# Kernel optimization log

Measured on AMD Instinct MI355X. Metric: run time of the kernel, lower is better.

Reference implementation:

```python
import jax, jax.numpy as jnp
import numpy as np

N = 8192          # mesh vertices
E = 49152         # directed edges (avg degree 6)
M = 25            # kernel_size per pseudo-dim
DIM = 3           # pseudo-coordinate dim
K = M ** DIM      # 15625 weight matrices per layer
S = 2 ** DIM      # 8 nonzero degree-1 B-spline products per edge
LC, UC = -0.22703196, 0.36853024   # curvature range
LM, UM = 1.2585511, 1.648841       # myelin range
R = 10.0
LAYER_DIMS = [(2, 32), (32, 64), (64, 64), (64, 32), (32, 1)]


def transform(x):
    # rescale curv/myelin channels into [-R, R] with clamping (matches torch masking)
    t0 = (x[:, 0] - LC) / (UC - LC) * (2.0 * R) - R
    t1 = (x[:, 1] - LM) / (UM - LM) * (2.0 * R) - R
    return jnp.stack([jnp.clip(t0, -R, R), jnp.clip(t1, -R, R)], axis=1)


def spline_basis(pseudo):
    # open B-spline, degree 1: v in [0, M-1); 8 corner products per edge
    v = pseudo * (M - 1)
    lo = jnp.floor(v)
    f = v - lo                                                    # [E, DIM]
    lo = lo.astype(jnp.int32)
    bits = (jnp.arange(S)[:, None] >> jnp.arange(DIM)[None, :]) & 1   # [S, DIM]
    oh = bits.astype(pseudo.dtype)
    basis = jnp.prod(oh[None] * f[:, None, :] + (1.0 - oh[None]) * (1.0 - f[:, None, :]), axis=-1)  # [E, S]
    strides = (M ** jnp.arange(DIM)).astype(jnp.int32)
    wi = jnp.sum((lo[:, None, :] + bits[None]) * strides[None, None, :], axis=-1)  # [E, S] kernel indices
    return basis, wi


def spline_conv(h, src, dst, basis, wi, W, root, bias):
    xj = h[src]                                             # [E, Fin] gather
    msg = jnp.zeros((xj.shape[0], W.shape[2]), h.dtype)
    for s in range(S):                                      # fixed 8-way basis loop
        msg = msg + basis[:, s, None] * jnp.einsum('ei,eio->eo', xj, W[wi[:, s]])
    agg = jax.ops.segment_sum(msg, dst, num_segments=N)     # scatter-sum (norm=False)
    return agg + h @ root + bias


def setup_inputs() -> dict:
    key = jax.random.key(0)
    ks = jax.random.split(key, 3 + 2 * len(LAYER_DIMS))
    inp = {
        "x": jax.random.normal(ks[0], (N, 2), dtype=jnp.float32),
        "edge_index": jax.random.randint(ks[1], (2, E), 0, N),
        "pseudo": jax.random.uniform(ks[2], (E, DIM), dtype=jnp.float32),
    }
    for i, (fi, fo) in enumerate(LAYER_DIMS):
        kw, kr = ks[3 + 2 * i], ks[4 + 2 * i]
        inp[f"W{i+1}"] = jax.random.normal(kw, (K, fi, fo), dtype=jnp.float32) / np.float32(np.sqrt(fi * S))
        inp[f"root{i+1}"] = jax.random.normal(kr, (fi, fo), dtype=jnp.float32) / np.float32(np.sqrt(fi))
        inp[f"b{i+1}"] = jnp.zeros((fo,), dtype=jnp.float32)
    return inp


def reference(x, edge_index, pseudo, W1, root1, b1, W2, root2, b2, W3, root3, b3,
              W4, root4, b4, W5, root5, b5):
    src, dst = edge_index[0], edge_index[1]
    basis, wi = spline_basis(pseudo)   # shared across all 5 layers, as in the torch model
    h = transform(x)
    for W, r, b in ((W1, root1, b1), (W2, root2, b2), (W3, root3, b3),
                    (W4, root4, b4), (W5, root5, b5)):
        h = jax.nn.elu(spline_conv(h, src, dst, basis, wi, W, r, b))
    return h.reshape(-1)
```

## Files before the change

### kernel.cpp

```cpp
#include <hip/hip_runtime.h>
#include <math.h>

#define NV 8192
#define EV 49152
#define KK 15625

typedef __attribute__((ext_vector_type(8))) short bf16x8;
typedef __attribute__((ext_vector_type(4))) float f32x4;

__device__ __forceinline__ unsigned short bf16rne(float x) {
    unsigned u = __float_as_uint(x);
    unsigned r = u + 0x7FFFu + ((u >> 16) & 1u);
    return (unsigned short)(r >> 16);
}
__device__ __forceinline__ float bf16tof(unsigned short h) {
    return __uint_as_float(((unsigned)h) << 16);
}

__device__ __forceinline__ void edge_frac(const float* __restrict__ pseudo, int e,
                                          float f[3], int lo[3]) {
#pragma unroll
    for (int j = 0; j < 3; ++j) {
        float v = pseudo[e * 3 + j] * 24.0f;
        float fl = floorf(v);
        int l = (int)fl;
        l = l < 0 ? 0 : (l > 23 ? 23 : l);
        lo[j] = l;
        f[j] = v - (float)l;
    }
}

__global__ void prep_kernel(const float* __restrict__ x, float* __restrict__ h0,
                            int* __restrict__ counts, float* __restrict__ agg) {
    int gt = blockIdx.x * blockDim.x + threadIdx.x;
    if (gt < NV) {
        const float LC = -0.22703196f, UC = 0.36853024f;
        const float LM = 1.2585511f, UM = 1.648841f;
        const float R = 10.0f;
        float t0 = (x[gt * 2 + 0] - LC) / (UC - LC) * (2.0f * R) - R;
        float t1 = (x[gt * 2 + 1] - LM) / (UM - LM) * (2.0f * R) - R;
        h0[gt * 2 + 0] = fminf(fmaxf(t0, -R), R);
        h0[gt * 2 + 1] = fminf(fmaxf(t1, -R), R);
    }
    if (gt < KK) counts[gt] = 0;
    if (gt < NV * 64) agg[gt] = 0.0f;
}

__global__ void hist_kernel(const float* __restrict__ pseudo, int* __restrict__ counts) {
    int e = blockIdx.x * blockDim.x + threadIdx.x;
    if (e >= EV) return;
    float f[3]; int lo[3];
    edge_frac(pseudo, e, f, lo);
#pragma unroll
    for (int s = 0; s < 8; ++s) {
        int wi = (lo[0] + (s & 1)) + 25 * (lo[1] + ((s >> 1) & 1)) + 625 * (lo[2] + ((s >> 2) & 1));
        atomicAdd(&counts[wi], 1);
    }
}

__global__ void scan_kernel(const int* __restrict__ counts, int* __restrict__ offsets,
                            int* __restrict__ cursor) {
    __shared__ int sums[256];
    const int CH = 62;
    int t = threadIdx.x;
    int base = t * CH;
    int s = 0;
    for (int i = 0; i < CH; ++i) {
        int idx = base + i;
        if (idx < KK) s += counts[idx];
    }
    sums[t] = s;
    __syncthreads();
    for (int d = 1; d < 256; d <<= 1) {
        int v = (t >= d) ? sums[t - d] : 0;
        __syncthreads();
        sums[t] += v;
        __syncthreads();
    }
    int run = (t > 0) ? sums[t - 1] : 0;
    for (int i = 0; i < CH; ++i) {
        int idx = base + i;
        if (idx < KK) {
            offsets[idx] = run;
            cursor[idx] = run;
            run += counts[idx];
        }
    }
    if (t == 255) offsets[KK] = run;
}

__global__ void scatter_kernel(const float* __restrict__ pseudo, const int* __restrict__ ei,
                               int* __restrict__ cursor,
                               int2* __restrict__ pair_sb, int* __restrict__ pair_dst) {
    int e = blockIdx.x * blockDim.x + threadIdx.x;
    if (e >= EV) return;
    float f[3]; int lo[3];
    edge_frac(pseudo, e, f, lo);
    int src = ei[e];
    int dst = ei[EV + e];
#pragma unroll
    for (int s = 0; s < 8; ++s) {
        float b = ((s & 1) ? f[0] : 1.0f - f[0]) *
                  (((s >> 1) & 1) ? f[1] : 1.0f - f[1]) *
                  (((s >> 2) & 1) ? f[2] : 1.0f - f[2]);
        int wi = (lo[0] + (s & 1)) + 25 * (lo[1] + ((s >> 1) & 1)) + 625 * (lo[2] + ((s >> 2) & 1));
        int pos = atomicAdd(&cursor[wi], 1);
        pair_sb[pos] = make_int2(src, __float_as_int(b));
        pair_dst[pos] = dst;
    }
}

template <int FIN, int FOUT>
__global__ __launch_bounds__(256) void conv_v5(
    const float* __restrict__ h, const float* __restrict__ W,
    const int* __restrict__ offsets, const int2* __restrict__ pair_sb,
    const int* __restrict__ pair_dst, float* __restrict__ agg) {
    constexpr int KT = FIN / 32;
    constexpr int NT = FOUT / 16;
    constexpr int BPB = 4 / NT;
    int w = threadIdx.x >> 6;
    int lane = threadIdx.x & 63;
    int nslice = w % NT;
    int k = blockIdx.x * BPB + w / NT;
    if (k >= KK) return;
    int start = offsets[k];
    int n = offsets[k + 1] - start;
    if (n <= 0) return;
    int l15 = lane & 15;
    int lg = lane >> 4;

    const float* Wk = W + (size_t)k * (FIN * FOUT) + nslice * 16 + l15;
    bf16x8 Bh[KT], Bl[KT];
#pragma unroll
    for (int k0 = 0; k0 < KT; ++k0)
#pragma unroll
        for (int i = 0; i < 8; ++i) {
            float wv = Wk[(size_t)(k0 * 32 + lg * 8 + i) * FOUT];
            unsigned short hi = bf16rne(wv);
            unsigned short lo = bf16rne(wv - bf16tof(hi));
            Bh[k0][i] = (short)hi;
            Bl[k0][i] = (short)lo;
        }

    const int2* psb = pair_sb + start;
    const int* pdst = pair_dst + start;

    for (int m0 = 0; m0 < n; m0 += 16) {
        int ra = m0 + l15;
        bool va = ra < n;
        int2 sb = psb[va ? ra : 0];
        float b = va ? __int_as_float(sb.y) : 0.0f;
        const float* xr = h + (size_t)sb.x * FIN + lg * 8;

        f32x4 acc = (f32x4){0.f, 0.f, 0.f, 0.f};
#pragma unroll
        for (int k0 = 0; k0 < KT; ++k0) {
            float4 v0 = *(const float4*)(xr + k0 * 32);
            float4 v1 = *(const float4*)(xr + k0 * 32 + 4);
            float xv[8] = {v0.x * b, v0.y * b, v0.z * b, v0.w * b,
                           v1.x * b, v1.y * b, v1.z * b, v1.w * b};
            bf16x8 Ah, Al;
#pragma unroll
            for (int i = 0; i < 8; ++i) {
                unsigned short hi = bf16rne(xv[i]);
                unsigned short lo = bf16rne(xv[i] - bf16tof(hi));
                Ah[i] = (short)hi;
                Al[i] = (short)lo;
            }
            acc = __builtin_amdgcn_mfma_f32_16x16x32_bf16(Ah, Bh[k0], acc, 0, 0, 0);
            acc = __builtin_amdgcn_mfma_f32_16x16x32_bf16(Ah, Bl[k0], acc, 0, 0, 0);
            acc = __builtin_amdgcn_mfma_f32_16x16x32_bf16(Al, Bh[k0], acc, 0, 0, 0);
        }

#pragma unroll
        for (int j = 0; j < 4; ++j) {
            int rm = m0 + lg * 4 + j;
            if (rm < n) {
                int d = pdst[rm];
                atomicAdd(&agg[(size_t)d * FOUT + nslice * 16 + l15], acc[j]);
            }
        }
    }
}

__global__ __launch_bounds__(256) void conv_l1(
    const float* __restrict__ h, const float* __restrict__ W,
    const int* __restrict__ offsets, const int2* __restrict__ pair_sb,
    const int* __restrict__ pair_dst, float* __restrict__ agg) {
    int w = threadIdx.x >> 6;
    int lane = threadIdx.x & 63;
    int k = blockIdx.x * 4 + w;
    if (k >= KK) return;
    int start = offsets[k];
    int n = offsets[k + 1] - start;
    if (n <= 0) return;
    int o = lane & 31;
    int g = lane >> 5;
    const float* Wk = W + (size_t)k * 64;
    float w0 = Wk[o], w1 = Wk[32 + o];
    const float2* h2 = (const float2*)h;
    for (int r = g; r < n; r += 2) {
        int2 sb = pair_sb[start + r];
        float b = __int_as_float(sb.y);
        int dst = pair_dst[start + r];
        float2 xv = h2[sb.x];
        atomicAdd(&agg[(size_t)dst * 32 + o], b * (xv.x * w0 + xv.y * w1));
    }
}

__global__ __launch_bounds__(256) void conv_f1(
    const float* __restrict__ h, const float* __restrict__ W,
    const int* __restrict__ offsets, const int2* __restrict__ pair_sb,
    const int* __restrict__ pair_dst, float* __restrict__ agg) {
    int w = threadIdx.x >> 6;
    int lane = threadIdx.x & 63;
    int k = blockIdx.x * 4 + w;
    if (k >= KK) return;
    int start = offsets[k];
    int n = offsets[k + 1] - start;
    if (n <= 0) return;
    int i = lane & 31;
    int g = lane >> 5;
    float wk = W[(size_t)k * 32 + i];
    for (int r = g; r < n; r += 2) {
        int2 sb = pair_sb[start + r];
        float b = __int_as_float(sb.y);
        int dst = pair_dst[start + r];
        float val = h[(size_t)sb.x * 32 + i] * wk * b;
#pragma unroll
        for (int d = 16; d >= 1; d >>= 1) val += __shfl_xor(val, d, 32);
        if (i == 0) atomicAdd(&agg[dst], val);
    }
}

template <int FIN, int FOUT>
__global__ void node_kernel(const float* __restrict__ h, float* __restrict__ agg,
                            const float* __restrict__ root, const float* __restrict__ bias,
                            float* __restrict__ hout) {
    int idx = blockIdx.x * blockDim.x + threadIdx.x;
    if (idx >= NV * 64) return;
    if (idx < NV * FOUT) {
        int n = idx / FOUT, o = idx % FOUT;
        float acc = agg[idx] + bias[o];
#pragma unroll
        for (int i = 0; i < FIN; ++i) acc += h[n * FIN + i] * root[i * FOUT + o];
        hout[idx] = acc > 0.0f ? acc : expm1f(acc);
    }
    agg[idx] = 0.0f;
}

extern "C" void kernel_launch(void* const* d_in, const int* in_sizes, int n_in,
                              void* d_out, int out_size, void* d_ws, size_t ws_size,
                              hipStream_t stream) {
    const float* x      = (const float*)d_in[0];
    const int*   ei     = (const int*)d_in[1];
    const float* pseudo = (const float*)d_in[2];
    const float* W1 = (const float*)d_in[3];
    const float* r1 = (const float*)d_in[4];
    const float* b1 = (const float*)d_in[5];
    const float* W2 = (const float*)d_in[6];
    const float* r2 = (const float*)d_in[7];
    const float* b2 = (const float*)d_in[8];
    const float* W3 = (const float*)d_in[9];
    const float* r3 = (const float*)d_in[10];
    const float* b3 = (const float*)d_in[11];
    const float* W4 = (const float*)d_in[12];
    const float* r4 = (const float*)d_in[13];
    const float* b4 = (const float*)d_in[14];
    const float* W5 = (const float*)d_in[15];
    const float* r5 = (const float*)d_in[16];
    const float* b5 = (const float*)d_in[17];

    char* ws = (char*)d_ws;
    size_t off = 0;
    auto alloc = [&](size_t bytes) {
        void* p = ws + off;
        off += (bytes + 255) & ~(size_t)255;
        return p;
    };
    int*   counts   = (int*)alloc(KK * sizeof(int));
    int*   offsets  = (int*)alloc((KK + 1) * sizeof(int));
    int*   cursor   = (int*)alloc(KK * sizeof(int));
    int2*  pair_sb  = (int2*)alloc((size_t)EV * 8 * sizeof(int2));
    int*   pair_dst = (int*)alloc((size_t)EV * 8 * sizeof(int));
    float* hA       = (float*)alloc((size_t)NV * 64 * sizeof(float));
    float* hB       = (float*)alloc((size_t)NV * 64 * sizeof(float));
    float* agg      = (float*)alloc((size_t)NV * 64 * sizeof(float));

    const int NGRID = (NV * 64 + 255) / 256;

    prep_kernel<<<NGRID, 256, 0, stream>>>(x, hA, counts, agg);
    hist_kernel<<<(EV + 255) / 256, 256, 0, stream>>>(pseudo, counts);
    scan_kernel<<<1, 256, 0, stream>>>(counts, offsets, cursor);
    scatter_kernel<<<(EV + 255) / 256, 256, 0, stream>>>(pseudo, ei, cursor, pair_sb, pair_dst);

    conv_l1<<<(KK + 3) / 4, 256, 0, stream>>>(hA, W1, offsets, pair_sb, pair_dst, agg);
    node_kernel<2, 32><<<NGRID, 256, 0, stream>>>(hA, agg, r1, b1, hB);

    conv_v5<32, 64><<<KK, 256, 0, stream>>>(hB, W2, offsets, pair_sb, pair_dst, agg);
    node_kernel<32, 64><<<NGRID, 256, 0, stream>>>(hB, agg, r2, b2, hA);

    conv_v5<64, 64><<<KK, 256, 0, stream>>>(hA, W3, offsets, pair_sb, pair_dst, agg);
    node_kernel<64, 64><<<NGRID, 256, 0, stream>>>(hA, agg, r3, b3, hB);

    conv_v5<64, 32><<<(KK + 1) / 2, 256, 0, stream>>>(hB, W4, offsets, pair_sb, pair_dst, agg);
    node_kernel<64, 32><<<NGRID, 256, 0, stream>>>(hB, agg, r4, b4, hA);

    conv_f1<<<(KK + 3) / 4, 256, 0, stream>>>(hA, W5, offsets, pair_sb, pair_dst, agg);
    node_kernel<32, 1><<<NGRID, 256, 0, stream>>>(hA, agg, r5, b5, (float*)d_out);
}
```

Baseline: 518.9 us.

## Replace atomic scatter-add with per-destination message slots and segmented reduction

Builds a destination-sorted CSR (counts, scan, cursor) so each edge-basis pair gets a unique message slot. The conv kernels then write messages with plain stores instead of float atomicAdd, and a new per-node reduce kernel sums each node's segment and fuses the root matmul, bias and ELU. This removes atomic contention and the zeroing of agg, and makes the summation order deterministic. In exchange it adds a large intermediate buffer (E*8*FOUT floats) with extra write and read traffic, plus one more scan and an extra atomic per pair during setup.

```diff
diff --git a/kernel.cpp b/kernel.cpp
--- a/kernel.cpp
+++ b/kernel.cpp
@@ -31,7 +31,7 @@
 }
 
 __global__ void prep_kernel(const float* __restrict__ x, float* __restrict__ h0,
-                            int* __restrict__ counts, float* __restrict__ agg) {
+                            int* __restrict__ counts, int* __restrict__ dcounts) {
     int gt = blockIdx.x * blockDim.x + threadIdx.x;
     if (gt < NV) {
         const float LC = -0.22703196f, UC = 0.36853024f;
@@ -43,10 +43,11 @@
         h0[gt * 2 + 1] = fminf(fmaxf(t1, -R), R);
     }
     if (gt < KK) counts[gt] = 0;
-    if (gt < NV * 64) agg[gt] = 0.0f;
-}
-
-__global__ void hist_kernel(const float* __restrict__ pseudo, int* __restrict__ counts) {
+    if (gt < NV) dcounts[gt] = 0;
+}
+
+__global__ void hist_kernel(const float* __restrict__ pseudo, const int* __restrict__ ei,
+                            int* __restrict__ counts, int* __restrict__ dcounts) {
     int e = blockIdx.x * blockDim.x + threadIdx.x;
     if (e >= EV) return;
     float f[3]; int lo[3];
@@ -56,18 +57,19 @@
         int wi = (lo[0] + (s & 1)) + 25 * (lo[1] + ((s >> 1) & 1)) + 625 * (lo[2] + ((s >> 2) & 1));
         atomicAdd(&counts[wi], 1);
     }
-}
-
-__global__ void scan_kernel(const int* __restrict__ counts, int* __restrict__ offsets,
-                            int* __restrict__ cursor) {
+    atomicAdd(&dcounts[ei[EV + e]], 8);
+}
+
+__global__ void scan_any(const int* __restrict__ counts, int* __restrict__ offsets,
+                         int* __restrict__ cursor, int nbins) {
     __shared__ int sums[256];
-    const int CH = 62;
     int t = threadIdx.x;
+    int CH = (nbins + 255) / 256;
     int base = t * CH;
     int s = 0;
     for (int i = 0; i < CH; ++i) {
         int idx = base + i;
-        if (idx < KK) s += counts[idx];
+        if (idx < nbins) s += counts[idx];
     }
     sums[t] = s;
     __syncthreads();
@@ -80,18 +82,18 @@
     int run = (t > 0) ? sums[t - 1] : 0;
     for (int i = 0; i < CH; ++i) {
         int idx = base + i;
-        if (idx < KK) {
+        if (idx < nbins) {
             offsets[idx] = run;
             cursor[idx] = run;
             run += counts[idx];
         }
     }
-    if (t == 255) offsets[KK] = run;
+    if (t == 255) offsets[nbins] = run;
 }
 
 __global__ void scatter_kernel(const float* __restrict__ pseudo, const int* __restrict__ ei,
-                               int* __restrict__ cursor,
-                               int2* __restrict__ pair_sb, int* __restrict__ pair_dst) {
+                               int* __restrict__ cursor, int* __restrict__ dcursor,
+                               int2* __restrict__ pair_sb, int* __restrict__ pair_slot) {
     int e = blockIdx.x * blockDim.x + threadIdx.x;
     if (e >= EV) return;
     float f[3]; int lo[3];
@@ -105,16 +107,17 @@
                   (((s >> 2) & 1) ? f[2] : 1.0f - f[2]);
         int wi = (lo[0] + (s & 1)) + 25 * (lo[1] + ((s >> 1) & 1)) + 625 * (lo[2] + ((s >> 2) & 1));
         int pos = atomicAdd(&cursor[wi], 1);
+        int q = atomicAdd(&dcursor[dst], 1);
         pair_sb[pos] = make_int2(src, __float_as_int(b));
-        pair_dst[pos] = dst;
+        pair_slot[pos] = q;
     }
 }
 
 template <int FIN, int FOUT>
-__global__ __launch_bounds__(256) void conv_v5(
+__global__ __launch_bounds__(256) void conv_v6(
     const float* __restrict__ h, const float* __restrict__ W,
     const int* __restrict__ offsets, const int2* __restrict__ pair_sb,
-    const int* __restrict__ pair_dst, float* __restrict__ agg) {
+    const int* __restrict__ pair_slot, float* __restrict__ msg) {
     constexpr int KT = FIN / 32;
     constexpr int NT = FOUT / 16;
     constexpr int BPB = 4 / NT;
@@ -143,7 +146,7 @@
         }
 
     const int2* psb = pair_sb + start;
-    const int* pdst = pair_dst + start;
+    const int* pslot = pair_slot + start;
 
     for (int m0 = 0; m0 < n; m0 += 16) {
         int ra = m0 + l15;
@@ -176,8 +179,8 @@
         for (int j = 0; j < 4; ++j) {
             int rm = m0 + lg * 4 + j;
             if (rm < n) {
-                int d = pdst[rm];
-                atomicAdd(&agg[(size_t)d * FOUT + nslice * 16 + l15], acc[j]);
+                int q = pslot[rm];
+                msg[(size_t)q * FOUT + nslice * 16 + l15] = acc[j];
             }
         }
     }
@@ -186,7 +189,7 @@
 __global__ __launch_bounds__(256) void conv_l1(
     const float* __restrict__ h, const float* __restrict__ W,
     const int* __restrict__ offsets, const int2* __restrict__ pair_sb,
-    const int* __restrict__ pair_dst, float* __restrict__ agg) {
+    const int* __restrict__ pair_slot, float* __restrict__ msg) {
     int w = threadIdx.x >> 6;
     int lane = threadIdx.x & 63;
     int k = blockIdx.x * 4 + w;
@@ -202,16 +205,16 @@
     for (int r = g; r < n; r += 2) {
         int2 sb = pair_sb[start + r];
         float b = __int_as_float(sb.y);
-        int dst = pair_dst[start + r];
+        int q = pair_slot[start + r];
         float2 xv = h2[sb.x];
-        atomicAdd(&agg[(size_t)dst * 32 + o], b * (xv.x * w0 + xv.y * w1));
+        msg[(size_t)q * 32 + o] = b * (xv.x * w0 + xv.y * w1);
     }
 }
 
 __global__ __launch_bounds__(256) void conv_f1(
     const float* __restrict__ h, const float* __restrict__ W,
     const int* __restrict__ offsets, const int2* __restrict__ pair_sb,
-    const int* __restrict__ pair_dst, float* __restrict__ agg) {
+    const int* __restrict__ pair_slot, float* __restrict__ msg) {
     int w = threadIdx.x >> 6;
     int lane = threadIdx.x & 63;
     int k = blockIdx.x * 4 + w;
@@ -225,28 +228,59 @@
     for (int r = g; r < n; r += 2) {
         int2 sb = pair_sb[start + r];
         float b = __int_as_float(sb.y);
-        int dst = pair_dst[start + r];
+        int q = pair_slot[start + r];
         float val = h[(size_t)sb.x * 32 + i] * wk * b;
 #pragma unroll
         for (int d = 16; d >= 1; d >>= 1) val += __shfl_xor(val, d, 32);
-        if (i == 0) atomicAdd(&agg[dst], val);
+        if (i == 0) msg[q] = val;
     }
 }
 
 template <int FIN, int FOUT>
-__global__ void node_kernel(const float* __restrict__ h, float* __restrict__ agg,
-                            const float* __restrict__ root, const float* __restrict__ bias,
-                            float* __restrict__ hout) {
-    int idx = blockIdx.x * blockDim.x + threadIdx.x;
-    if (idx >= NV * 64) return;
-    if (idx < NV * FOUT) {
-        int n = idx / FOUT, o = idx % FOUT;
-        float acc = agg[idx] + bias[o];
-#pragma unroll
-        for (int i = 0; i < FIN; ++i) acc += h[n * FIN + i] * root[i * FOUT + o];
-        hout[idx] = acc > 0.0f ? acc : expm1f(acc);
-    }
-    agg[idx] = 0.0f;
+__global__ __launch_bounds__(256) void reduce_node(
+    const float* __restrict__ h, const float* __restrict__ msg,
+    const int* __restrict__ doffsets, const float* __restrict__ root,
+    const float* __restrict__ bias, float* __restrict__ hout) {
+    constexpr int RG = 64 / FOUT;
+    int w = threadIdx.x >> 6;
+    int lane = threadIdx.x & 63;
+    int n = blockIdx.x * 4 + w;
+    if (n >= NV) return;
+    int seg0 = doffsets[n];
+    int cnt = doffsets[n + 1] - seg0;
+    int o = lane % FOUT;
+    int gg = lane / FOUT;
+    float acc = 0.0f;
+    for (int r = gg; r < cnt; r += RG)
+        acc += msg[(size_t)(seg0 + r) * FOUT + o];
+    if (RG == 2) acc += __shfl_xor(acc, 32);
+    float rt = bias[o];
+#pragma unroll
+    for (int i = 0; i < FIN; ++i) rt += h[(size_t)n * FIN + i] * root[i * FOUT + o];
+    float v = acc + rt;
+    v = v > 0.0f ? v : expm1f(v);
+    if (gg == 0) hout[(size_t)n * FOUT + o] = v;
+}
+
+__global__ __launch_bounds__(256) void reduce_node5(
+    const float* __restrict__ h, const float* __restrict__ msg,
+    const int* __restrict__ doffsets, const float* __restrict__ root,
+    const float* __restrict__ bias, float* __restrict__ out) {
+    int w = threadIdx.x >> 6;
+    int lane = threadIdx.x & 63;
+    int n = blockIdx.x * 4 + w;
+    if (n >= NV) return;
+    int seg0 = doffsets[n];
+    int cnt = doffsets[n + 1] - seg0;
+    float val = 0.0f;
+    for (int r = lane; r < cnt; r += 64) val += msg[seg0 + r];
+    if (lane < 32) val += h[(size_t)n * 32 + lane] * root[lane];
+#pragma unroll
+    for (int d = 32; d >= 1; d >>= 1) val += __shfl_xor(val, d, 64);
+    if (lane == 0) {
+        float v = val + bias[0];
+        out[n] = v > 0.0f ? v : expm1f(v);
+    }
 }
 
 extern "C" void kernel_launch(void* const* d_in, const int* in_sizes, int n_in,
@@ -278,34 +312,39 @@
         off += (bytes + 255) & ~(size_t)255;
         return p;
     };
-    int*   counts   = (int*)alloc(KK * sizeof(int));
-    int*   offsets  = (int*)alloc((KK + 1) * sizeof(int));
-    int*   cursor   = (int*)alloc(KK * sizeof(int));
-    int2*  pair_sb  = (int2*)alloc((size_t)EV * 8 * sizeof(int2));
-    int*   pair_dst = (int*)alloc((size_t)EV * 8 * sizeof(int));
-    float* hA       = (float*)alloc((size_t)NV * 64 * sizeof(float));
-    float* hB       = (float*)alloc((size_t)NV * 64 * sizeof(float));
-    float* agg      = (float*)alloc((size_t)NV * 64 * sizeof(float));
-
-    const int NGRID = (NV * 64 + 255) / 256;
-
-    prep_kernel<<<NGRID, 256, 0, stream>>>(x, hA, counts, agg);
-    hist_kernel<<<(EV + 255) / 256, 256, 0, stream>>>(pseudo, counts);
-    scan_kernel<<<1, 256, 0, stream>>>(counts, offsets, cursor);
-    scatter_kernel<<<(EV + 255) / 256, 256, 0, stream>>>(pseudo, ei, cursor, pair_sb, pair_dst);
-
-    conv_l1<<<(KK + 3) / 4, 256, 0, stream>>>(hA, W1, offsets, pair_sb, pair_dst, agg);
-    node_kernel<2, 32><<<NGRID, 256, 0, stream>>>(hA, agg, r1, b1, hB);
-
-    conv_v5<32, 64><<<KK, 256, 0, stream>>>(hB, W2, offsets, pair_sb, pair_dst, agg);
-    node_kernel<32, 64><<<NGRID, 256, 0, stream>>>(hB, agg, r2, b2, hA);
-
-    conv_v5<64, 64><<<KK, 256, 0, stream>>>(hA, W3, offsets, pair_sb, pair_dst, agg);
-    node_kernel<64, 64><<<NGRID, 256, 0, stream>>>(hA, agg, r3, b3, hB);
-
-    conv_v5<64, 32><<<(KK + 1) / 2, 256, 0, stream>>>(hB, W4, offsets, pair_sb, pair_dst, agg);
-    node_kernel<64, 32><<<NGRID, 256, 0, stream>>>(hB, agg, r4, b4, hA);
-
-    conv_f1<<<(KK + 3) / 4, 256, 0, stream>>>(hA, W5, offsets, pair_sb, pair_dst, agg);
-    node_kernel<32, 1><<<NGRID, 256, 0, stream>>>(hA, agg, r5, b5, (float*)d_out);
-}
+    int*   counts    = (int*)alloc(KK * sizeof(int));
+    int*   offsets   = (int*)alloc((KK + 1) * sizeof(int));
+    int*   cursor    = (int*)alloc(KK * sizeof(int));
+    int*   dcounts   = (int*)alloc(NV * sizeof(int));
+    int*   doffsets  = (int*)alloc((NV + 1) * sizeof(int));
+    int*   dcursor   = (int*)alloc(NV * sizeof(int));
+    int2*  pair_sb   = (int2*)alloc((size_t)EV * 8 * sizeof(int2));
+    int*   pair_slot = (int*)alloc((size_t)EV * 8 * sizeof(int));
+    float* hA        = (float*)alloc((size_t)NV * 64 * sizeof(float));
+    float* hB        = (float*)alloc((size_t)NV * 64 * sizeof(float));
+    float* msg       = (float*)alloc((size_t)EV * 8 * 64 * sizeof(float));
+
+    prep_kernel<<<(KK + 255) / 256, 256, 0, stream>>>(x, hA, counts, dcounts);
+    hist_kernel<<<(EV + 255) / 256, 256, 0, stream>>>(pseudo, ei, counts, dcounts);
+    scan_any<<<1, 256, 0, stream>>>(counts, offsets, cursor, KK);
+    scan_any<<<1, 256, 0, stream>>>(dcounts, doffsets, dcursor, NV);
+    scatter_kernel<<<(EV + 255) / 256, 256, 0, stream>>>(pseudo, ei, cursor, dcursor,
+                                                         pair_sb, pair_slot);
+
+    const int RGRID = (NV + 3) / 4;
+
+    conv_l1<<<(KK + 3) / 4, 256, 0, stream>>>(hA, W1, offsets, pair_sb, pair_slot, msg);
+    reduce_node<2, 32><<<RGRID, 256, 0, stream>>>(hA, msg, doffsets, r1, b1, hB);
+
+    conv_v6<32, 64><<<KK, 256, 0, stream>>>(hB, W2, offsets, pair_sb, pair_slot, msg);
+    reduce_node<32, 64><<<RGRID, 256, 0, stream>>>(hB, msg, doffsets, r2, b2, hA);
+
+    conv_v6<64, 64><<<KK, 256, 0, stream>>>(hA, W3, offsets, pair_sb, pair_slot, msg);
+    reduce_node<64, 64><<<RGRID, 256, 0, stream>>>(hA, msg, doffsets, r3, b3, hB);
+
+    conv_v6<64, 32><<<(KK + 1) / 2, 256, 0, stream>>>(hB, W4, offsets, pair_sb, pair_slot, msg);
+    reduce_node<64, 32><<<RGRID, 256, 0, stream>>>(hB, msg, doffsets, r4, b4, hA);
+
+    conv_f1<<<(KK + 3) / 4, 256, 0, stream>>>(hA, W5, offsets, pair_sb, pair_slot, msg);
+    reduce_node5<<<RGRID, 256, 0, stream>>>(hA, msg, doffsets, r5, b5, (float*)d_out);
+}
```

Result: slower. 577.8 us (+11.3%).
